# Performance work log

Measured on AMD Instinct MI355X. Metric: run time of the kernel, lower is better.

Reference implementation:

```python
import math
import jax, jax.numpy as jnp
import numpy as np

INPUT_DIM = 1024
OUTPUT_DIM = 1024
DEGREE = 8
EPS = 1.0


def setup_inputs() -> dict:
    key = jax.random.key(0)
    k1, k2 = jax.random.split(key)
    x = jax.random.normal(k1, (8192, INPUT_DIM), dtype=jnp.float32)
    std = 1.0 / (INPUT_DIM * (DEGREE + 1))
    hermite_coeffs = std * jax.random.normal(k2, (INPUT_DIM, OUTPUT_DIM, DEGREE + 1), dtype=jnp.float32)
    return {"x": x, "hermite_coeffs": hermite_coeffs}


def _hermite_basis(x):
    # x: [B, I] squashed input; returns [B, I, DEGREE+1] Hermite-function basis.
    pi_q = math.pi ** (-0.25)
    gauss = jnp.exp(-0.5 * x * x)
    h0 = pi_q * gauss
    hs = [h0]
    if DEGREE > 0:
        hs.append(math.sqrt(2.0) * pi_q * x * gauss)
    for i in range(2, DEGREE + 1):
        hs.append(math.sqrt(2.0 / i) * x * hs[i - 1] - math.sqrt((i - 1) / i) * hs[i - 2])
    return jnp.stack(hs, axis=-1)


def reference(x, hermite_coeffs):
    x = x.reshape(-1, INPUT_DIM)
    x = jnp.tanh(x) * (math.sqrt(2 * DEGREE + 1) + EPS)
    hermite = _hermite_basis(x)  # [B, I, D+1]
    y = jnp.einsum('bid,iod->bo', hermite, hermite_coeffs)
    return y.reshape(-1, OUTPUT_DIM)
```

## Files before the change

kernel.cpp:

```cpp
#include <hip/hip_runtime.h>

#define MDIM 8192
#define IDIM 1024
#define ODIM 1024
#define D1   9
#define KDIM (IDIM * D1)

typedef _Float16 half8   __attribute__((ext_vector_type(8)));
typedef float    float4v __attribute__((ext_vector_type(4)));

#define BSCALE 256.0f
#define INV_BSCALE (1.0f / 256.0f)
#define USCALE 5.123105625617661f
#define H0C 0.7511255444649425f
#define SQRT2 1.4142135623730951f

__device__ __forceinline__ half8 splat8(float f) {
    _Float16 h = (_Float16)f;
    return half8{h, h, h, h, h, h, h, h};
}

__device__ __forceinline__ void hermite9(float xv, float h[D1]) {
    float ax = fabsf(xv);
    float t  = __expf(-2.0f * ax);
    float th = (1.0f - t) / (1.0f + t);
    th = copysignf(th, xv);
    float u = th * USCALE;
    float g = __expf(-0.5f * u * u);
    h[0] = H0C * g;
    h[1] = SQRT2 * H0C * u * g;
    const float c1[D1] = {0.f, 0.f, 1.0f, 0.8164965809277260f, 0.7071067811865476f,
                          0.6324555320336759f, 0.5773502691896258f, 0.5345224838248488f, 0.5f};
    const float c2[D1] = {0.f, 0.f, 0.7071067811865476f, 0.8164965809277260f, 0.8660254037844386f,
                          0.8944271909999159f, 0.9128709291752769f, 0.9258200997725514f, 0.9354143466934853f};
#pragma unroll
    for (int d = 2; d < D1; ++d) h[d] = c1[d] * u * h[d - 1] - c2[d] * h[d - 2];
}

__global__ __launch_bounds__(256) void prep_all(const float* __restrict__ C,
                                                _Float16* __restrict__ Bt,
                                                const float* __restrict__ x,
                                                _Float16* __restrict__ U,
                                                _Float16* __restrict__ H0) {
    if (blockIdx.x < 1024) {
        __shared__ float lds[288 * 33];
        const int t  = threadIdx.x;
        const int ti = blockIdx.x & 31;
        const int to = blockIdx.x >> 5;
        const float* base = C + (size_t)ti * 32 * 9216 + (size_t)to * 32 * 9;
#pragma unroll
        for (int j = 0; j < 36; ++j) {
            int f   = t + 256 * j;
            int row = f / 288;
            int col = f - row * 288;
            lds[col * 33 + row] = base[(size_t)row * 9216 + col];
        }
        __syncthreads();
        _Float16* bb = Bt + (size_t)to * 32 * KDIM + ti * 32;
#pragma unroll
        for (int j = 0; j < 36; ++j) {
            int e   = t + 256 * j;
            int i   = e & 31;
            int odp = e >> 5;
            int ol  = odp / 9;
            int d   = odp - ol * 9;
            bb[(size_t)ol * KDIM + d * IDIM + i] = (_Float16)(lds[odp * 33 + i] * BSCALE);
        }
    } else {
        size_t t = (size_t)(blockIdx.x - 1024) * 256 + threadIdx.x;
        const float4* xp = (const float4*)(x + t * 8);
        float4 a0 = xp[0], a1 = xp[1];
        float xv[8] = {a0.x, a0.y, a0.z, a0.w, a1.x, a1.y, a1.z, a1.w};
        half8 uu, hh;
#pragma unroll
        for (int e = 0; e < 8; ++e) {
            float v  = xv[e];
            float t2 = __expf(-2.0f * fabsf(v));
            float th = (1.0f - t2) * __builtin_amdgcn_rcpf(1.0f + t2);
            float u  = copysignf(th, v) * USCALE;
            float g  = __expf(-0.5f * u * u);
            uu[e] = (_Float16)u;
            hh[e] = (_Float16)(H0C * g);
        }
        *(half8*)(U  + t * 8) = uu;
        *(half8*)(H0 + t * 8) = hh;
    }
}

__global__ __launch_bounds__(256, 2) void gemm_fused3(
    const _Float16* __restrict__ U,
    const _Float16* __restrict__ H0,
    const _Float16* __restrict__ Bt,
    float* __restrict__ out)
{
    const int tid = threadIdx.x;
    const int w = tid >> 6;
    const int l = tid & 63;
    const int bn = blockIdx.x;
    const int bm = blockIdx.y;

    __shared__ _Float16 Bs[2][128 * 64];

    const int lrow8 = l >> 3;
    const int kgrp  = (l & 7) ^ lrow8;
    const _Float16* Bg = Bt + ((size_t)(bn * 128 + w * 8 + lrow8) * KDIM + kgrp * 8);

    const int q   = l >> 4;
    const int m16 = l & 15;
    const int s3  = m16 & 7;
    const int wm  = w >> 1, wn = w & 1;

    half8 u2[4][2], hA[4][2], hB[4][2];
    const size_t arow = ((size_t)(bm * 128 + wm * 64 + m16)) << 10;
    const _Float16* Ubase = U  + arow + 8 * q;
    const _Float16* Hbase = H0 + arow + 8 * q;

    auto loadUH = [&](int kb) {
#pragma unroll
        for (int i = 0; i < 4; ++i)
#pragma unroll
            for (int ko = 0; ko < 2; ++ko) {
                size_t off = ((size_t)(i * 16) << 10) + kb + 32 * ko;
                u2[i][ko] = *(const half8*)(Ubase + off);
                hA[i][ko] = *(const half8*)(Hbase + off);
            }
    };

    float4v acc[4][4] = {};
    const half8 sq2v = splat8(SQRT2);

    constexpr float c1a[D1] = {0.f, 0.f, 1.0f, 0.8164965809277260f, 0.7071067811865476f,
                               0.6324555320336759f, 0.5773502691896258f, 0.5345224838248488f, 0.5f};
    constexpr float c2a[D1] = {0.f, 0.f, 0.7071067811865476f, 0.8164965809277260f, 0.8660254037844386f,
                               0.8944271909999159f, 0.9128709291752769f, 0.9258200997725514f, 0.9354143466934853f};

#pragma unroll
    for (int rr = 0; rr < 4; ++rr)
        __builtin_amdgcn_global_load_lds(
            (const __attribute__((address_space(1))) void*)(Bg + (size_t)(rr * 32) * KDIM),
            (__attribute__((address_space(3))) void*)((char*)&Bs[0][0] + (rr * 4 + w) * 1024),
            16, 0, 0);
    loadUH(0);

    for (int ib = 0; ib < 16; ++ib) {
        const int kbase = ib * 64;
#pragma unroll
        for (int d = 0; d < D1; ++d) {
            const int cur = (ib + d) & 1;
            const int nxt = cur ^ 1;

            __syncthreads();

            const bool has_next = (d < 8) || (ib < 15);
            if (has_next) {
                const int nkoff = (d == 8) ? (kbase + 64) : ((d + 1) * IDIM + kbase);
#pragma unroll
                for (int rr = 0; rr < 4; ++rr)
                    __builtin_amdgcn_global_load_lds(
                        (const __attribute__((address_space(1))) void*)(Bg + (size_t)(rr * 32) * KDIM + nkoff),
                        (__attribute__((address_space(3))) void*)((char*)&Bs[nxt][0] + (rr * 4 + w) * 1024),
                        16, 0, 0);
            }

            half8 af[4][2];
            if (d == 0) {
#pragma unroll
                for (int i = 0; i < 4; ++i)
#pragma unroll
                    for (int ko = 0; ko < 2; ++ko) {
                        hB[i][ko] = sq2v * u2[i][ko] * hA[i][ko];
                        af[i][ko] = hA[i][ko];
                    }
            } else if (d == 1) {
#pragma unroll
                for (int i = 0; i < 4; ++i)
#pragma unroll
                    for (int ko = 0; ko < 2; ++ko) af[i][ko] = hB[i][ko];
            } else if (d < 8) {
                const half8 c1v = splat8(c1a[d]);
                const half8 c2v = splat8(c2a[d]);
#pragma unroll
                for (int i = 0; i < 4; ++i)
#pragma unroll
                    for (int ko = 0; ko < 2; ++ko) {
                        half8 t  = u2[i][ko] * hB[i][ko];
                        half8 ht = c1v * t - c2v * hA[i][ko];
                        hA[i][ko] = hB[i][ko];
                        hB[i][ko] = ht;
                        af[i][ko] = ht;
                    }
            } else {
                const half8 c1v = splat8(c1a[8]);
                const half8 c2v = splat8(c2a[8]);
#pragma unroll
                for (int i = 0; i < 4; ++i)
#pragma unroll
                    for (int ko = 0; ko < 2; ++ko) {
                        half8 t = u2[i][ko] * hB[i][ko];
                        af[i][ko] = c1v * t - c2v * hA[i][ko];
                    }
                if (ib < 15) loadUH(kbase + 64);
            }

#pragma unroll
            for (int ko = 0; ko < 2; ++ko) {
                const int slot = (q + 4 * ko) ^ s3;
                half8 bf[4];
#pragma unroll
                for (int j = 0; j < 4; ++j)
                    bf[j] = *(const half8*)&Bs[cur][(wn * 64 + j * 16 + m16) * 64 + slot * 8];
#pragma unroll
                for (int i = 0; i < 4; ++i)
#pragma unroll
                    for (int j = 0; j < 4; ++j)
                        acc[i][j] = __builtin_amdgcn_mfma_f32_16x16x32_f16(af[i][ko], bf[j], acc[i][j], 0, 0, 0);
            }
        }
    }

#pragma unroll
    for (int i = 0; i < 4; ++i) {
        int row = bm * 128 + wm * 64 + i * 16 + q * 4;
#pragma unroll
        for (int j = 0; j < 4; ++j) {
            int col = bn * 128 + wn * 64 + j * 16 + m16;
            float* op = out + (size_t)row * ODIM + col;
#pragma unroll
            for (int r2 = 0; r2 < 4; ++r2)
                op[(size_t)r2 * ODIM] = acc[i][j][r2] * INV_BSCALE;
        }
    }
}

__global__ void naive_kernel(const float* __restrict__ x, const float* __restrict__ C,
                             float* __restrict__ out) {
    __shared__ float hb[IDIM * D1];
    int b = blockIdx.x;
    int tid = threadIdx.x;
    for (int i = tid; i < IDIM; i += 256) {
        float h[D1];
        hermite9(x[(size_t)b * IDIM + i], h);
#pragma unroll
        for (int d = 0; d < D1; ++d) hb[i * D1 + d] = h[d];
    }
    __syncthreads();
    for (int o = tid; o < ODIM; o += 256) {
        float acc = 0.f;
        for (int i = 0; i < IDIM; ++i) {
            const float* cp = C + ((size_t)i * ODIM + o) * D1;
            const float* hp = hb + i * D1;
#pragma unroll
            for (int d = 0; d < D1; ++d) acc += hp[d] * cp[d];
        }
        out[(size_t)b * ODIM + o] = acc;
    }
}

extern "C" void kernel_launch(void* const* d_in, const int* in_sizes, int n_in,
                              void* d_out, int out_size, void* d_ws, size_t ws_size,
                              hipStream_t stream) {
    const float* x      = (const float*)d_in[0];
    const float* coeffs = (const float*)d_in[1];
    float* out = (float*)d_out;

    const size_t bt_bytes = (size_t)ODIM * KDIM * sizeof(_Float16);
    const size_t u_bytes  = (size_t)MDIM * IDIM * sizeof(_Float16);

    if (ws_size >= bt_bytes + 2 * u_bytes) {
        _Float16* Bt = (_Float16*)d_ws;
        _Float16* Uv = (_Float16*)((char*)d_ws + bt_bytes);
        _Float16* H0 = (_Float16*)((char*)d_ws + bt_bytes + u_bytes);
        hipLaunchKernelGGL(prep_all, dim3(1024 + (MDIM * IDIM) / 2048), dim3(256), 0, stream,
                           coeffs, Bt, x, Uv, H0);
        hipLaunchKernelGGL(gemm_fused3, dim3(8, 64), dim3(256), 0, stream, Uv, H0, Bt, out);
    } else {
        hipLaunchKernelGGL(naive_kernel, dim3(MDIM), dim3(256), 0, stream, x, coeffs, out);
    }
}
```

Before: 284.8 us.

## Load B fragments directly into registers, dropping LDS staging and barriers

Replaces the LDS double-buffered B tile (global_load_lds plus __syncthreads per step) with per-lane direct global loads of B fragments into a two-deep register buffer, with the ib loop unrolled by two so buffer indices stay static. The aim is to remove the barriers and the LDS round-trip. The cost is that each B element is now fetched by both wm-halves of the block, so global and L2 traffic rises, and register pressure grows with the extra 16 half8 buffers. The coefficient tables also move to __constant__ memory.

```diff
diff --git a/kernel.cpp b/kernel.cpp
--- a/kernel.cpp
+++ b/kernel.cpp
@@ -19,6 +19,11 @@
     _Float16 h = (_Float16)f;
     return half8{h, h, h, h, h, h, h, h};
 }
+
+__constant__ float c1a[D1] = {0.f, 0.f, 1.0f, 0.8164965809277260f, 0.7071067811865476f,
+                              0.6324555320336759f, 0.5773502691896258f, 0.5345224838248488f, 0.5f};
+__constant__ float c2a[D1] = {0.f, 0.f, 0.7071067811865476f, 0.8164965809277260f, 0.8660254037844386f,
+                              0.8944271909999159f, 0.9128709291752769f, 0.9258200997725514f, 0.9354143466934853f};
 
 __device__ __forceinline__ void hermite9(float xv, float h[D1]) {
     float ax = fabsf(xv);
@@ -29,12 +34,8 @@
     float g = __expf(-0.5f * u * u);
     h[0] = H0C * g;
     h[1] = SQRT2 * H0C * u * g;
-    const float c1[D1] = {0.f, 0.f, 1.0f, 0.8164965809277260f, 0.7071067811865476f,
-                          0.6324555320336759f, 0.5773502691896258f, 0.5345224838248488f, 0.5f};
-    const float c2[D1] = {0.f, 0.f, 0.7071067811865476f, 0.8164965809277260f, 0.8660254037844386f,
-                          0.8944271909999159f, 0.9128709291752769f, 0.9258200997725514f, 0.9354143466934853f};
-#pragma unroll
-    for (int d = 2; d < D1; ++d) h[d] = c1[d] * u * h[d - 1] - c2[d] * h[d - 2];
+#pragma unroll
+    for (int d = 2; d < D1; ++d) h[d] = c1a[d] * u * h[d - 1] - c2a[d] * h[d - 2];
 }
 
 __global__ __launch_bounds__(256) void prep_all(const float* __restrict__ C,
@@ -87,7 +88,7 @@
     }
 }
 
-__global__ __launch_bounds__(256, 2) void gemm_fused3(
+__global__ __launch_bounds__(256, 2) void gemm_reg(
     const _Float16* __restrict__ U,
     const _Float16* __restrict__ H0,
     const _Float16* __restrict__ Bt,
@@ -99,21 +100,23 @@
     const int bn = blockIdx.x;
     const int bm = blockIdx.y;
 
-    __shared__ _Float16 Bs[2][128 * 64];
-
-    const int lrow8 = l >> 3;
-    const int kgrp  = (l & 7) ^ lrow8;
-    const _Float16* Bg = Bt + ((size_t)(bn * 128 + w * 8 + lrow8) * KDIM + kgrp * 8);
-
     const int q   = l >> 4;
     const int m16 = l & 15;
-    const int s3  = m16 & 7;
     const int wm  = w >> 1, wn = w & 1;
 
-    half8 u2[4][2], hA[4][2], hB[4][2];
+    const _Float16* Brow[4];
+#pragma unroll
+    for (int j = 0; j < 4; ++j)
+        Brow[j] = Bt + (size_t)(bn * 128 + wn * 64 + j * 16 + m16) * KDIM + 8 * q;
+
     const size_t arow = ((size_t)(bm * 128 + wm * 64 + m16)) << 10;
     const _Float16* Ubase = U  + arow + 8 * q;
     const _Float16* Hbase = H0 + arow + 8 * q;
+
+    half8 u2[4][2], hA[4][2], hB[4][2];
+    half8 bbuf[2][4][2];
+    float4v acc[4][4] = {};
+    const half8 sq2v = splat8(SQRT2);
 
     auto loadUH = [&](int kb) {
 #pragma unroll
@@ -126,97 +129,80 @@
             }
     };
 
-    float4v acc[4][4] = {};
-    const half8 sq2v = splat8(SQRT2);
-
-    constexpr float c1a[D1] = {0.f, 0.f, 1.0f, 0.8164965809277260f, 0.7071067811865476f,
-                               0.6324555320336759f, 0.5773502691896258f, 0.5345224838248488f, 0.5f};
-    constexpr float c2a[D1] = {0.f, 0.f, 0.7071067811865476f, 0.8164965809277260f, 0.8660254037844386f,
-                               0.8944271909999159f, 0.9128709291752769f, 0.9258200997725514f, 0.9354143466934853f};
-
-#pragma unroll
-    for (int rr = 0; rr < 4; ++rr)
-        __builtin_amdgcn_global_load_lds(
-            (const __attribute__((address_space(1))) void*)(Bg + (size_t)(rr * 32) * KDIM),
-            (__attribute__((address_space(3))) void*)((char*)&Bs[0][0] + (rr * 4 + w) * 1024),
-            16, 0, 0);
+#define HSTEP(D, CUR, NXT, HN, NK)                                                        \
+    {                                                                                     \
+        if (HN) {                                                                         \
+            _Pragma("unroll")                                                             \
+            for (int j = 0; j < 4; ++j) {                                                 \
+                bbuf[NXT][j][0] = *(const half8*)(Brow[j] + (NK));                        \
+                bbuf[NXT][j][1] = *(const half8*)(Brow[j] + (NK) + 32);                   \
+            }                                                                             \
+        }                                                                                 \
+        _Pragma("unroll")                                                                 \
+        for (int i = 0; i < 4; ++i) {                                                     \
+            half8 af0, af1;                                                               \
+            if ((D) == 0) {                                                               \
+                hB[i][0] = sq2v * u2[i][0] * hA[i][0];                                    \
+                hB[i][1] = sq2v * u2[i][1] * hA[i][1];                                    \
+                af0 = hA[i][0]; af1 = hA[i][1];                                           \
+            } else if ((D) == 1) {                                                        \
+                af0 = hB[i][0]; af1 = hB[i][1];                                           \
+            } else if ((D) < 8) {                                                         \
+                const half8 c1v = splat8(c1a[(D)]);                                       \
+                const half8 c2v = splat8(c2a[(D)]);                                       \
+                af0 = c1v * (u2[i][0] * hB[i][0]) - c2v * hA[i][0];                       \
+                af1 = c1v * (u2[i][1] * hB[i][1]) - c2v * hA[i][1];                       \
+                hA[i][0] = hB[i][0]; hB[i][0] = af0;                                      \
+                hA[i][1] = hB[i][1]; hB[i][1] = af1;                                      \
+            } else {                                                                      \
+                const half8 c1v = splat8(c1a[8]);                                         \
+                const half8 c2v = splat8(c2a[8]);                                         \
+                af0 = c1v * (u2[i][0] * hB[i][0]) - c2v * hA[i][0];                       \
+                af1 = c1v * (u2[i][1] * hB[i][1]) - c2v * hA[i][1];                       \
+            }                                                                             \
+            _Pragma("unroll")                                                             \
+            for (int j = 0; j < 4; ++j) {                                                 \
+                acc[i][j] = __builtin_amdgcn_mfma_f32_16x16x32_f16(af0, bbuf[CUR][j][0],  \
+                                                                   acc[i][j], 0, 0, 0);   \
+                acc[i][j] = __builtin_amdgcn_mfma_f32_16x16x32_f16(af1, bbuf[CUR][j][1],  \
+                                                                   acc[i][j], 0, 0, 0);   \
+            }                                                                             \
+        }                                                                                 \
+    }
+
     loadUH(0);
-
-    for (int ib = 0; ib < 16; ++ib) {
-        const int kbase = ib * 64;
-#pragma unroll
-        for (int d = 0; d < D1; ++d) {
-            const int cur = (ib + d) & 1;
-            const int nxt = cur ^ 1;
-
-            __syncthreads();
-
-            const bool has_next = (d < 8) || (ib < 15);
-            if (has_next) {
-                const int nkoff = (d == 8) ? (kbase + 64) : ((d + 1) * IDIM + kbase);
-#pragma unroll
-                for (int rr = 0; rr < 4; ++rr)
-                    __builtin_amdgcn_global_load_lds(
-                        (const __attribute__((address_space(1))) void*)(Bg + (size_t)(rr * 32) * KDIM + nkoff),
-                        (__attribute__((address_space(3))) void*)((char*)&Bs[nxt][0] + (rr * 4 + w) * 1024),
-                        16, 0, 0);
+#pragma unroll
+    for (int j = 0; j < 4; ++j) {
+        bbuf[0][j][0] = *(const half8*)(Brow[j]);
+        bbuf[0][j][1] = *(const half8*)(Brow[j] + 32);
+    }
+
+    for (int ib2 = 0; ib2 < 16; ib2 += 2) {
+        const int kb0 = ib2 * 64;
+        const int kb1 = kb0 + 64;
+#pragma unroll
+        for (int d = 0; d < 9; ++d) {
+            if (d < 8) {
+                const int nk = (d + 1) * IDIM + kb0;
+                if (d & 1) { HSTEP(d, 1, 0, true, nk) } else { HSTEP(d, 0, 1, true, nk) }
+            } else {
+                HSTEP(8, 0, 1, true, kb1)
+                loadUH(kb1);
             }
-
-            half8 af[4][2];
-            if (d == 0) {
-#pragma unroll
-                for (int i = 0; i < 4; ++i)
-#pragma unroll
-                    for (int ko = 0; ko < 2; ++ko) {
-                        hB[i][ko] = sq2v * u2[i][ko] * hA[i][ko];
-                        af[i][ko] = hA[i][ko];
-                    }
-            } else if (d == 1) {
-#pragma unroll
-                for (int i = 0; i < 4; ++i)
-#pragma unroll
-                    for (int ko = 0; ko < 2; ++ko) af[i][ko] = hB[i][ko];
-            } else if (d < 8) {
-                const half8 c1v = splat8(c1a[d]);
-                const half8 c2v = splat8(c2a[d]);
-#pragma unroll
-                for (int i = 0; i < 4; ++i)
-#pragma unroll
-                    for (int ko = 0; ko < 2; ++ko) {
-                        half8 t  = u2[i][ko] * hB[i][ko];
-                        half8 ht = c1v * t - c2v * hA[i][ko];
-                        hA[i][ko] = hB[i][ko];
-                        hB[i][ko] = ht;
-                        af[i][ko] = ht;
-                    }
+        }
+#pragma unroll
+        for (int d = 0; d < 9; ++d) {
+            if (d < 8) {
+                const int nk = (d + 1) * IDIM + kb1;
+                if (d & 1) { HSTEP(d, 0, 1, true, nk) } else { HSTEP(d, 1, 0, true, nk) }
             } else {
-                const half8 c1v = splat8(c1a[8]);
-                const half8 c2v = splat8(c2a[8]);
-#pragma unroll
-                for (int i = 0; i < 4; ++i)
-#pragma unroll
-                    for (int ko = 0; ko < 2; ++ko) {
-                        half8 t = u2[i][ko] * hB[i][ko];
-                        af[i][ko] = c1v * t - c2v * hA[i][ko];
-                    }
-                if (ib < 15) loadUH(kbase + 64);
+                const bool hn = (ib2 < 14);
+                HSTEP(8, 1, 0, hn, kb1 + 64)
+                if (hn) loadUH(kb1 + 64);
             }
-
-#pragma unroll
-            for (int ko = 0; ko < 2; ++ko) {
-                const int slot = (q + 4 * ko) ^ s3;
-                half8 bf[4];
-#pragma unroll
-                for (int j = 0; j < 4; ++j)
-                    bf[j] = *(const half8*)&Bs[cur][(wn * 64 + j * 16 + m16) * 64 + slot * 8];
-#pragma unroll
-                for (int i = 0; i < 4; ++i)
-#pragma unroll
-                    for (int j = 0; j < 4; ++j)
-                        acc[i][j] = __builtin_amdgcn_mfma_f32_16x16x32_f16(af[i][ko], bf[j], acc[i][j], 0, 0, 0);
-            }
-        }
-    }
+        }
+    }
+#undef HSTEP
 
 #pragma unroll
     for (int i = 0; i < 4; ++i) {
@@ -272,7 +258,7 @@
         _Float16* H0 = (_Float16*)((char*)d_ws + bt_bytes + u_bytes);
         hipLaunchKernelGGL(prep_all, dim3(1024 + (MDIM * IDIM) / 2048), dim3(256), 0, stream,
                            coeffs, Bt, x, Uv, H0);
-        hipLaunchKernelGGL(gemm_fused3, dim3(8, 64), dim3(256), 0, stream, Uv, H0, Bt, out);
+        hipLaunchKernelGGL(gemm_reg, dim3(8, 64), dim3(256), 0, stream, Uv, H0, Bt, out);
     } else {
         hipLaunchKernelGGL(naive_kernel, dim3(MDIM), dim3(256), 0, stream, x, coeffs, out);
     }
```

New measurement: 449.6 us. 57.8% more time.
